# Optimization experiments

Measured on AMD Instinct MI355X. Metric: run time of the kernel, lower is better.

The kernel has to match this reference:

```python
import jax, jax.numpy as jnp
import numpy as np


def setup_inputs() -> dict:
    key = jax.random.key(0)
    ks = jax.random.split(key, 4)
    B, T, D, H = 64, 512, 512, 1024
    return {
        "x": jax.random.normal(ks[0], (B, T, D), dtype=jnp.float32),
        "kz": jax.random.normal(ks[1], (D, H), dtype=jnp.float32) * (1.0 / np.sqrt(D)),
        "kr": jax.random.normal(ks[2], (D, H), dtype=jnp.float32) * (1.0 / np.sqrt(D)),
        "kh": jax.random.normal(ks[3], (D, H), dtype=jnp.float32) * (1.0 / np.sqrt(D)),
        "mz": jnp.ones((H,), dtype=jnp.float32),
        "mr": jnp.ones((H,), dtype=jnp.float32),
        "br": jnp.zeros((H,), dtype=jnp.float32),
        "bz": jnp.zeros((H,), dtype=jnp.float32),
    }


def reference(x, kz, kr, kh, mz, mr, br, bz):
    B, T, D = x.shape
    H = kz.shape[1]
    # Precompute input projections for all timesteps (batched GEMMs),
    # identical math to per-step matmuls in the original cell.
    xz = jnp.einsum("btd,dh->bth", x, kz)  # [B,T,H]
    xr = jnp.einsum("btd,dh->bth", x, kr)
    xh = jnp.einsum("btd,dh->bth", x, kh)

    def step(h, inp):
        xz_t, xr_t, xh_t = inp  # each [B,H]
        r = jnp.tanh(xr_t + h * mr + br) + 1.0
        z = jax.nn.sigmoid(xz_t + h * mz + bz)
        h_new = z * h + (1.0 - z) * jnp.tanh(xh_t + r * h)
        return h_new, h_new

    h0 = jnp.zeros((B, H), dtype=x.dtype)
    # scan over time axis: move T to leading dim
    xs = (jnp.swapaxes(xz, 0, 1), jnp.swapaxes(xr, 0, 1), jnp.swapaxes(xh, 0, 1))
    _, ys = jax.lax.scan(step, h0, xs)  # ys: [T,B,H]
    return jnp.swapaxes(ys, 0, 1)  # [B,T,H]
```

## Files before the change

### kernel.cpp

```cpp
#include <hip/hip_runtime.h>
#include <hip/hip_bf16.h>
#include <math.h>


#define M_DIM 32768
#define K_DIM 512
#define H_DIM 1024
#define N3    3072

typedef _Float16 half8v __attribute__((ext_vector_type(8)));
typedef _Float16 half4v __attribute__((ext_vector_type(4)));
typedef float f32x4 __attribute__((ext_vector_type(4)));

__device__ __forceinline__ f32x4 mfma16(half8v a, half8v b, f32x4 c) {
    return __builtin_amdgcn_mfma_f32_16x16x32_f16(a, b, c, 0, 0, 0);
}

__device__ __forceinline__ void load_lds16(const void* g, void* l) {
    __builtin_amdgcn_global_load_lds(
        (const __attribute__((address_space(1))) void*)g,
        (__attribute__((address_space(3))) void*)l, 16, 0, 0);
}

__global__ __launch_bounds__(256) void convert_x(
    const float4* __restrict__ x4, half4v* __restrict__ hi4,
    half4v* __restrict__ lo4, int n4)
{
    int i = blockIdx.x * 256 + threadIdx.x;
    if (i >= n4) return;
    float4 v = x4[i];
    half4v h, lo;
    h.x = (_Float16)v.x; lo.x = (_Float16)(v.x - (float)h.x);
    h.y = (_Float16)v.y; lo.y = (_Float16)(v.y - (float)h.y);
    h.z = (_Float16)v.z; lo.z = (_Float16)(v.z - (float)h.z);
    h.w = (_Float16)v.w; lo.w = (_Float16)(v.w - (float)h.w);
    hi4[i] = h; lo4[i] = lo;
}

__global__ __launch_bounds__(256) void convert_wt(
    const float* __restrict__ kz, const float* __restrict__ kr,
    const float* __restrict__ kh, _Float16* __restrict__ wth,
    _Float16* __restrict__ wtl)
{
    int gid = blockIdx.x * 256 + threadIdx.x;
    int k = gid & (K_DIM - 1);
    int n = (gid >> 9) & (H_DIM - 1);
    int wsel = gid >> 19;
    const float* s = (wsel == 0) ? kz : ((wsel == 1) ? kr : kh);
    float v = s[(size_t)k * H_DIM + n];
    _Float16 h = (_Float16)v;
    wth[gid] = h;
    wtl[gid] = (_Float16)(v - (float)h);
}

__global__ __launch_bounds__(256) void gemm_mfma_split(
    const _Float16* __restrict__ Ahi, const _Float16* __restrict__ Alo,
    const _Float16* __restrict__ Bthi, const _Float16* __restrict__ Btlo,
    float* __restrict__ XZ, float* __restrict__ XR, float* __restrict__ OUT)
{
    __shared__ _Float16 Ah[128 * 32];
    __shared__ _Float16 Al[128 * 32];
    __shared__ _Float16 Bh[128 * 32];
    __shared__ _Float16 Bl[128 * 32];

    const int tid = threadIdx.x;
    const int w = tid >> 6, l = tid & 63;
    const int l15 = l & 15, quad = l >> 4;
    const int bx = blockIdx.x, by = blockIdx.y;
    const long m0 = (long)by * 128;
    const long n0 = (long)bx * 128;

    f32x4 acc[4][4] = {};

    const int s1 = tid, s2 = tid + 256;
    const long aoff1 = (m0 + (s1 >> 2)) * K_DIM + (s1 & 3) * 8;
    const long aoff2 = (m0 + (s2 >> 2)) * K_DIM + (s2 & 3) * 8;
    const long boff1 = (n0 + (s1 >> 2)) * K_DIM + (s1 & 3) * 8;
    const long boff2 = (n0 + (s2 >> 2)) * K_DIM + (s2 & 3) * 8;

    const _Float16* a1 = Ahi + aoff1;  const _Float16* a2 = Ahi + aoff2;
    const _Float16* q1 = Alo + aoff1;  const _Float16* q2 = Alo + aoff2;
    const _Float16* b1 = Bthi + boff1; const _Float16* b2 = Bthi + boff2;
    const _Float16* c1 = Btlo + boff1; const _Float16* c2 = Btlo + boff2;

    _Float16* ldsA1 = &Ah[w * 512]; _Float16* ldsA2 = &Ah[2048 + w * 512];
    _Float16* ldsQ1 = &Al[w * 512]; _Float16* ldsQ2 = &Al[2048 + w * 512];
    _Float16* ldsB1 = &Bh[w * 512]; _Float16* ldsB2 = &Bh[2048 + w * 512];
    _Float16* ldsC1 = &Bl[w * 512]; _Float16* ldsC2 = &Bl[2048 + w * 512];

    const int wm = (w >> 1) * 64, wn = (w & 1) * 64;

    for (int kk = 0; kk < K_DIM / 32; ++kk) {
        load_lds16(a1, ldsA1); load_lds16(a2, ldsA2);
        load_lds16(q1, ldsQ1); load_lds16(q2, ldsQ2);
        load_lds16(b1, ldsB1); load_lds16(b2, ldsB2);
        load_lds16(c1, ldsC1); load_lds16(c2, ldsC2);
        a1 += 32; a2 += 32; q1 += 32; q2 += 32;
        b1 += 32; b2 += 32; c1 += 32; c2 += 32;
        __syncthreads();

        half8v afh[4], afl[4], bfh[4], bfl[4];
#pragma unroll
        for (int mi = 0; mi < 4; ++mi) {
            int row = (wm + mi * 16 + l15) * 32 + quad * 8;
            afh[mi] = *(const half8v*)&Ah[row];
            afl[mi] = *(const half8v*)&Al[row];
        }
#pragma unroll
        for (int ni = 0; ni < 4; ++ni) {
            int row = (wn + ni * 16 + l15) * 32 + quad * 8;
            bfh[ni] = *(const half8v*)&Bh[row];
            bfl[ni] = *(const half8v*)&Bl[row];
        }
#pragma unroll
        for (int mi = 0; mi < 4; ++mi)
#pragma unroll
            for (int ni = 0; ni < 4; ++ni) {
                acc[mi][ni] = mfma16(afh[mi], bfh[ni], acc[mi][ni]);
                acc[mi][ni] = mfma16(afh[mi], bfl[ni], acc[mi][ni]);
                acc[mi][ni] = mfma16(afl[mi], bfh[ni], acc[mi][ni]);
            }
        __syncthreads();
    }

    float* dst = (bx < 8) ? XZ : ((bx < 16) ? XR : OUT);
    const long nl = (long)(bx & 7) * 128 + wn + l15;
#pragma unroll
    for (int mi = 0; mi < 4; ++mi) {
        const long m = m0 + wm + mi * 16 + quad * 4;
#pragma unroll
        for (int ni = 0; ni < 4; ++ni) {
            float* p = dst + m * H_DIM + nl + ni * 16;
#pragma unroll
            for (int i = 0; i < 4; ++i)
                p[(long)i * H_DIM] = acc[mi][ni][i];
        }
    }
}

#define BM 128
#define BN 128
#define BK 8
__global__ __launch_bounds__(256) void gemm_f32(
    const float* __restrict__ A, const float* __restrict__ B,
    float* __restrict__ C, int M, int N, int K)
{
    __shared__ float As[BK][BM];
    __shared__ float Bs[BK][BN];
    const int tid = threadIdx.x;
    const int bm = blockIdx.y * BM, bn = blockIdx.x * BN;
    const int tx = tid & 15, ty = tid >> 4;
    float acc[8][8];
#pragma unroll
    for (int i = 0; i < 8; i++)
#pragma unroll
        for (int j = 0; j < 8; j++) acc[i][j] = 0.f;
    const int a_row = tid >> 1, a_k = (tid & 1) * 4;
    const int b_row = tid >> 5, b_col = (tid & 31) * 4;
    const float* Aptr = A + (size_t)(bm + a_row) * K + a_k;
    const float* Bptr = B + (size_t)b_row * N + bn + b_col;
    for (int k0 = 0; k0 < K; k0 += BK) {
        float4 av = *(const float4*)(Aptr + k0);
        float4 bv = *(const float4*)(Bptr + (size_t)k0 * N);
        As[a_k + 0][a_row] = av.x; As[a_k + 1][a_row] = av.y;
        As[a_k + 2][a_row] = av.z; As[a_k + 3][a_row] = av.w;
        *(float4*)&Bs[b_row][b_col] = bv;
        __syncthreads();
#pragma unroll
        for (int kk = 0; kk < BK; kk++) {
            float4 a0 = *(const float4*)&As[kk][ty * 8];
            float4 a1 = *(const float4*)&As[kk][ty * 8 + 4];
            float4 b0 = *(const float4*)&Bs[kk][tx * 8];
            float4 b1 = *(const float4*)&Bs[kk][tx * 8 + 4];
            float a[8] = {a0.x, a0.y, a0.z, a0.w, a1.x, a1.y, a1.z, a1.w};
            float b[8] = {b0.x, b0.y, b0.z, b0.w, b1.x, b1.y, b1.z, b1.w};
#pragma unroll
            for (int i = 0; i < 8; i++)
#pragma unroll
                for (int j = 0; j < 8; j++)
                    acc[i][j] = fmaf(a[i], b[j], acc[i][j]);
        }
        __syncthreads();
    }
    float* Cptr = C + (size_t)(bm + ty * 8) * N + bn + tx * 8;
#pragma unroll
    for (int i = 0; i < 8; i++) {
        float4 c0 = {acc[i][0], acc[i][1], acc[i][2], acc[i][3]};
        float4 c1 = {acc[i][4], acc[i][5], acc[i][6], acc[i][7]};
        *(float4*)(Cptr + (size_t)i * N)     = c0;
        *(float4*)(Cptr + (size_t)i * N + 4) = c1;
    }
}

__device__ __forceinline__ float fast_tanh(float x) {
    return 1.0f - 2.0f / (__expf(2.0f * x) + 1.0f);
}
__device__ __forceinline__ float fast_sigmoid(float x) {
    return 1.0f / (1.0f + __expf(-x));
}

__global__ __launch_bounds__(256) void scan_kernel(
    const float* __restrict__ XZ, const float* __restrict__ XR,
    float* __restrict__ OUT,
    const float* __restrict__ mz, const float* __restrict__ mr,
    const float* __restrict__ br, const float* __restrict__ bz)
{
    const int gid = blockIdx.x * blockDim.x + threadIdx.x;
    const int b = gid >> 10;
    const int h = gid & (H_DIM - 1);

    const float mzv = mz[h], mrv = mr[h], brv = br[h], bzv = bz[h];
    float hs = 0.f;
    size_t idx = (size_t)b * 512 * H_DIM + h;

    float cz[8], cr[8], ch[8];
#pragma unroll
    for (int j = 0; j < 8; ++j) {
        cz[j] = XZ[idx + (size_t)j * H_DIM];
        cr[j] = XR[idx + (size_t)j * H_DIM];
        ch[j] = OUT[idx + (size_t)j * H_DIM];
    }
    for (int t0 = 0; t0 < 512; t0 += 8) {
        float nz[8], nr[8], nh[8];
        const bool more = (t0 + 8) < 512;
        const size_t nidx = idx + 8ul * H_DIM;
        if (more) {
#pragma unroll
            for (int j = 0; j < 8; ++j) {
                nz[j] = XZ[nidx + (size_t)j * H_DIM];
                nr[j] = XR[nidx + (size_t)j * H_DIM];
                nh[j] = OUT[nidx + (size_t)j * H_DIM];
            }
        }
#pragma unroll
        for (int j = 0; j < 8; ++j) {
            const float r = fast_tanh(fmaf(hs, mrv, cr[j]) + brv) + 1.0f;
            const float z = fast_sigmoid(fmaf(hs, mzv, cz[j]) + bzv);
            const float hn = fmaf(z, hs, (1.0f - z) * fast_tanh(fmaf(r, hs, ch[j])));
            OUT[idx + (size_t)j * H_DIM] = hn;
            hs = hn;
        }
        idx = nidx;
        if (more) {
#pragma unroll
            for (int j = 0; j < 8; ++j) { cz[j] = nz[j]; cr[j] = nr[j]; ch[j] = nh[j]; }
        }
    }
}

extern "C" void kernel_launch(void* const* d_in, const int* in_sizes, int n_in,
                              void* d_out, int out_size, void* d_ws, size_t ws_size,
                              hipStream_t stream) {
    const float* x  = (const float*)d_in[0];
    const float* kz = (const float*)d_in[1];
    const float* kr = (const float*)d_in[2];
    const float* kh = (const float*)d_in[3];
    const float* mz = (const float*)d_in[4];
    const float* mr = (const float*)d_in[5];
    const float* br = (const float*)d_in[6];
    const float* bz = (const float*)d_in[7];
    float* out = (float*)d_out;

    char* ws = (char*)d_ws;
    float* XZ = (float*)ws;
    float* XR = (float*)(ws + 134217728ul);
    _Float16* XHI = (_Float16*)(ws + 268435456ul);
    _Float16* XLO = (_Float16*)(ws + 301989888ul);
    _Float16* WTH = (_Float16*)(ws + 335544320ul);
    _Float16* WTL = (_Float16*)(ws + 338690048ul);
    const size_t need = 341835776ul;

    if (ws_size >= need) {
        int n4 = M_DIM * K_DIM / 4;
        convert_x<<<n4 / 256, 256, 0, stream>>>(
            (const float4*)x, (half4v*)XHI, (half4v*)XLO, n4);
        convert_wt<<<(3 * H_DIM * K_DIM) / 256, 256, 0, stream>>>(
            kz, kr, kh, WTH, WTL);
        dim3 grid(N3 / 128, M_DIM / 128);
        gemm_mfma_split<<<grid, 256, 0, stream>>>(
            XHI, XLO, WTH, WTL, XZ, XR, out);
    } else {
        dim3 grid(H_DIM / BN, M_DIM / BM);
        gemm_f32<<<grid, 256, 0, stream>>>(x, kz, XZ,  M_DIM, H_DIM, K_DIM);
        gemm_f32<<<grid, 256, 0, stream>>>(x, kr, XR,  M_DIM, H_DIM, K_DIM);
        gemm_f32<<<grid, 256, 0, stream>>>(x, kh, out, M_DIM, H_DIM, K_DIM);
    }

    scan_kernel<<<(64 * H_DIM) / 256, 256, 0, stream>>>(
        XZ, XR, out, mz, mr, br, bz);
}
```

Measured before the change: 613.4 us.

## Swizzle GEMM LDS layout, remap blocks for XCD locality, deepen scan prefetch

The split-fp16 GEMM now packs the hi and lo halves into combined 64-wide LDS rows with an XOR swizzle, to cut bank conflicts on fragment reads. It also launches a 1D grid and remaps block ids so that consecutive blocks on each of 8 groups cover nearby tiles, aiming for better L2 reuse across XCDs. Separately, the scan kernel's register prefetch depth is raised from 8 to 16 timesteps to hide more memory latency, at the cost of more registers and possibly lower occupancy.

```diff
diff --git a/kernel.cpp b/kernel.cpp
--- a/kernel.cpp
+++ b/kernel.cpp
@@ -58,59 +58,64 @@
     const _Float16* __restrict__ Bthi, const _Float16* __restrict__ Btlo,
     float* __restrict__ XZ, float* __restrict__ XR, float* __restrict__ OUT)
 {
-    __shared__ _Float16 Ah[128 * 32];
-    __shared__ _Float16 Al[128 * 32];
-    __shared__ _Float16 Bh[128 * 32];
-    __shared__ _Float16 Bl[128 * 32];
+    __shared__ _Float16 AT[128 * 64];
+    __shared__ _Float16 BT[128 * 64];
 
     const int tid = threadIdx.x;
     const int w = tid >> 6, l = tid & 63;
     const int l15 = l & 15, quad = l >> 4;
-    const int bx = blockIdx.x, by = blockIdx.y;
+
+    const int nblk = blockIdx.x;
+    const int swz = (nblk & 7) * 768 + (nblk >> 3);
+    const int by = swz / 24;
+    const int bx = swz - by * 24;
     const long m0 = (long)by * 128;
     const long n0 = (long)bx * 128;
 
     f32x4 acc[4][4] = {};
 
-    const int s1 = tid, s2 = tid + 256;
-    const long aoff1 = (m0 + (s1 >> 2)) * K_DIM + (s1 & 3) * 8;
-    const long aoff2 = (m0 + (s2 >> 2)) * K_DIM + (s2 & 3) * 8;
-    const long boff1 = (n0 + (s1 >> 2)) * K_DIM + (s1 & 3) * 8;
-    const long boff2 = (n0 + (s2 >> 2)) * K_DIM + (s2 & 3) * 8;
-
-    const _Float16* a1 = Ahi + aoff1;  const _Float16* a2 = Ahi + aoff2;
-    const _Float16* q1 = Alo + aoff1;  const _Float16* q2 = Alo + aoff2;
-    const _Float16* b1 = Bthi + boff1; const _Float16* b2 = Bthi + boff2;
-    const _Float16* c1 = Btlo + boff1; const _Float16* c2 = Btlo + boff2;
-
-    _Float16* ldsA1 = &Ah[w * 512]; _Float16* ldsA2 = &Ah[2048 + w * 512];
-    _Float16* ldsQ1 = &Al[w * 512]; _Float16* ldsQ2 = &Al[2048 + w * 512];
-    _Float16* ldsB1 = &Bh[w * 512]; _Float16* ldsB2 = &Bh[2048 + w * 512];
-    _Float16* ldsC1 = &Bl[w * 512]; _Float16* ldsC2 = &Bl[2048 + w * 512];
+    const _Float16* gsrc[8];
+    _Float16* ldst[8];
+#pragma unroll
+    for (int i = 0; i < 8; ++i) {
+        const int sb = w * 64 + (i & 3) * 256;
+        const int s  = sb + l;
+        const int r  = s >> 3;
+        const int o2 = ((s & 7) ^ (r & 7)) << 4;
+        const int part  = o2 >> 6;
+        const int khalf = ((o2 >> 4) & 3) * 8;
+        const bool isB = (i >= 4);
+        const long grow = (isB ? n0 : m0) + r;
+        const _Float16* base =
+            isB ? (part ? Btlo : Bthi) : (part ? Alo : Ahi);
+        gsrc[i] = base + grow * K_DIM + khalf;
+        ldst[i] = (isB ? BT : AT) + sb * 8;
+    }
 
     const int wm = (w >> 1) * 64, wn = (w & 1) * 64;
 
     for (int kk = 0; kk < K_DIM / 32; ++kk) {
-        load_lds16(a1, ldsA1); load_lds16(a2, ldsA2);
-        load_lds16(q1, ldsQ1); load_lds16(q2, ldsQ2);
-        load_lds16(b1, ldsB1); load_lds16(b2, ldsB2);
-        load_lds16(c1, ldsC1); load_lds16(c2, ldsC2);
-        a1 += 32; a2 += 32; q1 += 32; q2 += 32;
-        b1 += 32; b2 += 32; c1 += 32; c2 += 32;
+#pragma unroll
+        for (int i = 0; i < 8; ++i) {
+            load_lds16(gsrc[i], ldst[i]);
+            gsrc[i] += 32;
+        }
         __syncthreads();
 
         half8v afh[4], afl[4], bfh[4], bfl[4];
 #pragma unroll
         for (int mi = 0; mi < 4; ++mi) {
-            int row = (wm + mi * 16 + l15) * 32 + quad * 8;
-            afh[mi] = *(const half8v*)&Ah[row];
-            afl[mi] = *(const half8v*)&Al[row];
+            const int r = wm + mi * 16 + l15;
+            const int off = (quad ^ (r & 7)) * 8;
+            afh[mi] = *(const half8v*)&AT[r * 64 + off];
+            afl[mi] = *(const half8v*)&AT[r * 64 + (off ^ 32)];
         }
 #pragma unroll
         for (int ni = 0; ni < 4; ++ni) {
-            int row = (wn + ni * 16 + l15) * 32 + quad * 8;
-            bfh[ni] = *(const half8v*)&Bh[row];
-            bfl[ni] = *(const half8v*)&Bl[row];
+            const int r = wn + ni * 16 + l15;
+            const int off = (quad ^ (r & 7)) * 8;
+            bfh[ni] = *(const half8v*)&BT[r * 64 + off];
+            bfl[ni] = *(const half8v*)&BT[r * 64 + (off ^ 32)];
         }
 #pragma unroll
         for (int mi = 0; mi < 4; ++mi)
@@ -213,27 +218,27 @@
     float hs = 0.f;
     size_t idx = (size_t)b * 512 * H_DIM + h;
 
-    float cz[8], cr[8], ch[8];
-#pragma unroll
-    for (int j = 0; j < 8; ++j) {
+    float cz[16], cr[16], ch[16];
+#pragma unroll
+    for (int j = 0; j < 16; ++j) {
         cz[j] = XZ[idx + (size_t)j * H_DIM];
         cr[j] = XR[idx + (size_t)j * H_DIM];
         ch[j] = OUT[idx + (size_t)j * H_DIM];
     }
-    for (int t0 = 0; t0 < 512; t0 += 8) {
-        float nz[8], nr[8], nh[8];
-        const bool more = (t0 + 8) < 512;
-        const size_t nidx = idx + 8ul * H_DIM;
+    for (int t0 = 0; t0 < 512; t0 += 16) {
+        float nz[16], nr[16], nh[16];
+        const bool more = (t0 + 16) < 512;
+        const size_t nidx = idx + 16ul * H_DIM;
         if (more) {
 #pragma unroll
-            for (int j = 0; j < 8; ++j) {
+            for (int j = 0; j < 16; ++j) {
                 nz[j] = XZ[nidx + (size_t)j * H_DIM];
                 nr[j] = XR[nidx + (size_t)j * H_DIM];
                 nh[j] = OUT[nidx + (size_t)j * H_DIM];
             }
         }
 #pragma unroll
-        for (int j = 0; j < 8; ++j) {
+        for (int j = 0; j < 16; ++j) {
             const float r = fast_tanh(fmaf(hs, mrv, cr[j]) + brv) + 1.0f;
             const float z = fast_sigmoid(fmaf(hs, mzv, cz[j]) + bzv);
             const float hn = fmaf(z, hs, (1.0f - z) * fast_tanh(fmaf(r, hs, ch[j])));
@@ -243,7 +248,7 @@
         idx = nidx;
         if (more) {
 #pragma unroll
-            for (int j = 0; j < 8; ++j) { cz[j] = nz[j]; cr[j] = nr[j]; ch[j] = nh[j]; }
+            for (int j = 0; j < 16; ++j) { cz[j] = nz[j]; cr[j] = nr[j]; ch[j] = nh[j]; }
         }
     }
 }
@@ -276,8 +281,7 @@
             (const float4*)x, (half4v*)XHI, (half4v*)XLO, n4);
         convert_wt<<<(3 * H_DIM * K_DIM) / 256, 256, 0, stream>>>(
             kz, kr, kh, WTH, WTL);
-        dim3 grid(N3 / 128, M_DIM / 128);
-        gemm_mfma_split<<<grid, 256, 0, stream>>>(
+        gemm_mfma_split<<<6144, 256, 0, stream>>>(
             XHI, XLO, WTH, WTL, XZ, XR, out);
     } else {
         dim3 grid(H_DIM / BN, M_DIM / BM);
```

New measurement: 612.2 us. Within noise of the previous version (-0.2%).

## Store GEMM projections time-contiguous per (b,h) and vectorize scan loads

Applied to the files above, without the earlier changes.

The GEMM epilogue now writes the projections in a [B,H,T] layout, so each scan thread reads its own time series with contiguous float4 loads instead of strided per-step loads. The scan kernel folds the bias and gate constants into the preloaded values, prefetches 32 steps at a time, and replaces the divisions with rcp plus one Newton step. The weight conversion now transposes through shared memory to get coalesced accesses. This path needs an extra 128MB workspace buffer, and the transposed epilogue writes 16-byte chunks that are strided by 2KB.

```diff
diff --git a/kernel.cpp b/kernel.cpp
--- a/kernel.cpp
+++ b/kernel.cpp
@@ -37,22 +37,47 @@
     hi4[i] = h; lo4[i] = lo;
 }
 
-__global__ __launch_bounds__(256) void convert_wt(
+__global__ __launch_bounds__(256) void convert_wt_t(
     const float* __restrict__ kz, const float* __restrict__ kr,
     const float* __restrict__ kh, _Float16* __restrict__ wth,
     _Float16* __restrict__ wtl)
 {
-    int gid = blockIdx.x * 256 + threadIdx.x;
-    int k = gid & (K_DIM - 1);
-    int n = (gid >> 9) & (H_DIM - 1);
-    int wsel = gid >> 19;
-    const float* s = (wsel == 0) ? kz : ((wsel == 1) ? kr : kh);
-    float v = s[(size_t)k * H_DIM + n];
-    _Float16 h = (_Float16)v;
-    wth[gid] = h;
-    wtl[gid] = (_Float16)(v - (float)h);
-}
-
+    __shared__ float lds[64][65];
+    const int bid = blockIdx.x;
+    const int w = bid >> 7;
+    const int rem = bid & 127;
+    const int k0 = (rem >> 4) * 64;
+    const int n0 = (rem & 15) * 64;
+    const int tid = threadIdx.x;
+    const float* s = (w == 0) ? kz : ((w == 1) ? kr : kh);
+
+#pragma unroll
+    for (int r = 0; r < 4; ++r) {
+        const int kk = (tid >> 4) + r * 16;
+        const int nn = (tid & 15) * 4;
+        float4 v = *(const float4*)&s[(size_t)(k0 + kk) * H_DIM + n0 + nn];
+        lds[kk][nn + 0] = v.x; lds[kk][nn + 1] = v.y;
+        lds[kk][nn + 2] = v.z; lds[kk][nn + 3] = v.w;
+    }
+    __syncthreads();
+#pragma unroll
+    for (int r = 0; r < 4; ++r) {
+        const int nr = (tid >> 4) + r * 16;
+        const int kb = (tid & 15) * 4;
+        half4v hi, lo;
+#pragma unroll
+        for (int i = 0; i < 4; ++i) {
+            float v = lds[kb + i][nr];
+            _Float16 h = (_Float16)v;
+            hi[i] = h; lo[i] = (_Float16)(v - (float)h);
+        }
+        const size_t o = ((size_t)(w * H_DIM + n0 + nr)) * K_DIM + k0 + kb;
+        *(half4v*)&wth[o] = hi;
+        *(half4v*)&wtl[o] = lo;
+    }
+}
+
+template<bool TR>
 __global__ __launch_bounds__(256) void gemm_mfma_split(
     const _Float16* __restrict__ Ahi, const _Float16* __restrict__ Alo,
     const _Float16* __restrict__ Bthi, const _Float16* __restrict__ Btlo,
@@ -123,17 +148,32 @@
         __syncthreads();
     }
 
-    float* dst = (bx < 8) ? XZ : ((bx < 16) ? XR : OUT);
-    const long nl = (long)(bx & 7) * 128 + wn + l15;
-#pragma unroll
-    for (int mi = 0; mi < 4; ++mi) {
-        const long m = m0 + wm + mi * 16 + quad * 4;
-#pragma unroll
-        for (int ni = 0; ni < 4; ++ni) {
-            float* p = dst + m * H_DIM + nl + ni * 16;
-#pragma unroll
-            for (int i = 0; i < 4; ++i)
-                p[(long)i * H_DIM] = acc[mi][ni][i];
+    if (!TR) {
+        float* dst = (bx < 8) ? XZ : ((bx < 16) ? XR : OUT);
+        const long nl = (long)(bx & 7) * 128 + wn + l15;
+#pragma unroll
+        for (int mi = 0; mi < 4; ++mi) {
+            const long m = m0 + wm + mi * 16 + quad * 4;
+#pragma unroll
+            for (int ni = 0; ni < 4; ++ni) {
+                float* p = dst + m * H_DIM + nl + ni * 16;
+#pragma unroll
+                for (int i = 0; i < 4; ++i)
+                    p[(long)i * H_DIM] = acc[mi][ni][i];
+            }
+        }
+    } else {
+        float* dst = (bx < 8) ? XZ : ((bx < 16) ? XR : OUT);
+#pragma unroll
+        for (int mi = 0; mi < 4; ++mi) {
+            const long m = m0 + wm + mi * 16 + quad * 4;
+            const long b = m >> 9;
+            const long t = m & 511;
+#pragma unroll
+            for (int ni = 0; ni < 4; ++ni) {
+                const long n = (long)(bx & 7) * 128 + wn + ni * 16 + l15;
+                *(f32x4*)&dst[((size_t)(b * H_DIM + n) << 9) + t] = acc[mi][ni];
+            }
         }
     }
 }
@@ -192,11 +232,86 @@
     }
 }
 
-__device__ __forceinline__ float fast_tanh(float x) {
-    return 1.0f - 2.0f / (__expf(2.0f * x) + 1.0f);
-}
-__device__ __forceinline__ float fast_sigmoid(float x) {
-    return 1.0f / (1.0f + __expf(-x));
+__device__ __forceinline__ float vrcp_nr(float d) {
+    float r = __builtin_amdgcn_rcpf(d);
+    return r * fmaf(-d, r, 2.0f);
+}
+
+__global__ __launch_bounds__(256) void scan_t(
+    const float* __restrict__ XZt, const float* __restrict__ XRt,
+    const float* __restrict__ XHt, float* __restrict__ out,
+    const float* __restrict__ mz, const float* __restrict__ mr,
+    const float* __restrict__ br, const float* __restrict__ bz)
+{
+    const int gid = blockIdx.x * blockDim.x + threadIdx.x;
+    const int b = gid >> 10;
+    const int h = gid & (H_DIM - 1);
+
+    const float mzK = -mz[h];
+    const float mrK = -2.0f * mr[h];
+    const float bzK = -bz[h];
+    const float brK = -2.0f * br[h];
+    float hs = 0.f;
+
+    const size_t sbase = ((size_t)(b * H_DIM + h)) << 9;
+    const float4* pz = (const float4*)(XZt + sbase);
+    const float4* pr = (const float4*)(XRt + sbase);
+    const float4* ph = (const float4*)(XHt + sbase);
+    float* const po = out + ((size_t)b << 19) + h;
+
+    float cz[32], cr[32], ch[32];
+#pragma unroll
+    for (int q = 0; q < 8; ++q) {
+        float4 vz = pz[q], vr = pr[q], vh = ph[q];
+        cz[q*4+0] = bzK - vz.x; cz[q*4+1] = bzK - vz.y;
+        cz[q*4+2] = bzK - vz.z; cz[q*4+3] = bzK - vz.w;
+        cr[q*4+0] = fmaf(-2.0f, vr.x, brK); cr[q*4+1] = fmaf(-2.0f, vr.y, brK);
+        cr[q*4+2] = fmaf(-2.0f, vr.z, brK); cr[q*4+3] = fmaf(-2.0f, vr.w, brK);
+        ch[q*4+0] = -2.0f * vh.x; ch[q*4+1] = -2.0f * vh.y;
+        ch[q*4+2] = -2.0f * vh.z; ch[q*4+3] = -2.0f * vh.w;
+    }
+    for (int t0 = 0; t0 < 512; t0 += 32) {
+        float4 nz4[8], nr4[8], nh4[8];
+        const bool more = (t0 + 32) < 512;
+        if (more) {
+            const int b4 = (t0 + 32) >> 2;
+#pragma unroll
+            for (int q = 0; q < 8; ++q) {
+                nz4[q] = pz[b4 + q]; nr4[q] = pr[b4 + q]; nh4[q] = ph[b4 + q];
+            }
+        }
+        float* pout = po + ((size_t)t0 << 10);
+#pragma unroll
+        for (int j = 0; j < 32; ++j) {
+            const float u1   = fmaf(hs, mrK, cr[j]);
+            const float uz   = fmaf(hs, mzK, cz[j]);
+            const float hsK2 = -4.0f * hs;
+            const float e1 = __expf(u1);
+            const float s1 = vrcp_nr(e1 + 1.0f);
+            const float ez = __expf(uz);
+            const float sz = vrcp_nr(ez + 1.0f);
+            const float u2 = fmaf(s1, hsK2, ch[j]);
+            const float e2 = __expf(u2);
+            const float s2 = vrcp_nr(e2 + 1.0f);
+            const float th = fmaf(2.0f, s2, -1.0f);
+            const float hn = fmaf(sz, hs - th, th);
+            *pout = hn; pout += H_DIM;
+            hs = hn;
+        }
+        if (more) {
+#pragma unroll
+            for (int q = 0; q < 8; ++q) {
+                cz[q*4+0] = bzK - nz4[q].x; cz[q*4+1] = bzK - nz4[q].y;
+                cz[q*4+2] = bzK - nz4[q].z; cz[q*4+3] = bzK - nz4[q].w;
+                cr[q*4+0] = fmaf(-2.0f, nr4[q].x, brK);
+                cr[q*4+1] = fmaf(-2.0f, nr4[q].y, brK);
+                cr[q*4+2] = fmaf(-2.0f, nr4[q].z, brK);
+                cr[q*4+3] = fmaf(-2.0f, nr4[q].w, brK);
+                ch[q*4+0] = -2.0f * nh4[q].x; ch[q*4+1] = -2.0f * nh4[q].y;
+                ch[q*4+2] = -2.0f * nh4[q].z; ch[q*4+3] = -2.0f * nh4[q].w;
+            }
+        }
+    }
 }
 
 __global__ __launch_bounds__(256) void scan_kernel(
@@ -209,41 +324,57 @@
     const int b = gid >> 10;
     const int h = gid & (H_DIM - 1);
 
-    const float mzv = mz[h], mrv = mr[h], brv = br[h], bzv = bz[h];
+    const float mzK = -mz[h];
+    const float mrK = -2.0f * mr[h];
+    const float bzK = -bz[h];
+    const float brK = -2.0f * br[h];
     float hs = 0.f;
     size_t idx = (size_t)b * 512 * H_DIM + h;
 
-    float cz[8], cr[8], ch[8];
-#pragma unroll
-    for (int j = 0; j < 8; ++j) {
-        cz[j] = XZ[idx + (size_t)j * H_DIM];
-        cr[j] = XR[idx + (size_t)j * H_DIM];
-        ch[j] = OUT[idx + (size_t)j * H_DIM];
-    }
-    for (int t0 = 0; t0 < 512; t0 += 8) {
-        float nz[8], nr[8], nh[8];
-        const bool more = (t0 + 8) < 512;
-        const size_t nidx = idx + 8ul * H_DIM;
+    float cz[16], cr[16], ch[16];
+#pragma unroll
+    for (int j = 0; j < 16; ++j) {
+        cz[j] = bzK - XZ[idx + (size_t)j * H_DIM];
+        cr[j] = fmaf(-2.0f, XR[idx + (size_t)j * H_DIM], brK);
+        ch[j] = -2.0f * OUT[idx + (size_t)j * H_DIM];
+    }
+    for (int t0 = 0; t0 < 512; t0 += 16) {
+        float nz[16], nr[16], nh[16];
+        const bool more = (t0 + 16) < 512;
+        const size_t nidx = idx + 16ul * H_DIM;
         if (more) {
 #pragma unroll
-            for (int j = 0; j < 8; ++j) {
+            for (int j = 0; j < 16; ++j) {
                 nz[j] = XZ[nidx + (size_t)j * H_DIM];
                 nr[j] = XR[nidx + (size_t)j * H_DIM];
                 nh[j] = OUT[nidx + (size_t)j * H_DIM];
             }
         }
 #pragma unroll
-        for (int j = 0; j < 8; ++j) {
-            const float r = fast_tanh(fmaf(hs, mrv, cr[j]) + brv) + 1.0f;
-            const float z = fast_sigmoid(fmaf(hs, mzv, cz[j]) + bzv);
-            const float hn = fmaf(z, hs, (1.0f - z) * fast_tanh(fmaf(r, hs, ch[j])));
+        for (int j = 0; j < 16; ++j) {
+            const float u1   = fmaf(hs, mrK, cr[j]);
+            const float uz   = fmaf(hs, mzK, cz[j]);
+            const float hsK2 = -4.0f * hs;
+            const float e1 = __expf(u1);
+            const float s1 = vrcp_nr(e1 + 1.0f);
+            const float ez = __expf(uz);
+            const float sz = vrcp_nr(ez + 1.0f);
+            const float u2 = fmaf(s1, hsK2, ch[j]);
+            const float e2 = __expf(u2);
+            const float s2 = vrcp_nr(e2 + 1.0f);
+            const float th = fmaf(2.0f, s2, -1.0f);
+            const float hn = fmaf(sz, hs - th, th);
             OUT[idx + (size_t)j * H_DIM] = hn;
             hs = hn;
         }
         idx = nidx;
         if (more) {
 #pragma unroll
-            for (int j = 0; j < 8; ++j) { cz[j] = nz[j]; cr[j] = nr[j]; ch[j] = nh[j]; }
+            for (int j = 0; j < 16; ++j) {
+                cz[j] = bzK - nz[j];
+                cr[j] = fmaf(-2.0f, nr[j], brK);
+                ch[j] = -2.0f * nh[j];
+            }
         }
     }
 }
@@ -262,30 +393,52 @@
     float* out = (float*)d_out;
 
     char* ws = (char*)d_ws;
-    float* XZ = (float*)ws;
-    float* XR = (float*)(ws + 134217728ul);
-    _Float16* XHI = (_Float16*)(ws + 268435456ul);
-    _Float16* XLO = (_Float16*)(ws + 301989888ul);
-    _Float16* WTH = (_Float16*)(ws + 335544320ul);
-    _Float16* WTL = (_Float16*)(ws + 338690048ul);
-    const size_t need = 341835776ul;
-
-    if (ws_size >= need) {
-        int n4 = M_DIM * K_DIM / 4;
+    const int n4 = M_DIM * K_DIM / 4;
+
+    const size_t need_t = 476053504ul;
+    const size_t need_o = 341835776ul;
+
+    if (ws_size >= need_t) {
+        float* XZt = (float*)ws;
+        float* XRt = (float*)(ws + 134217728ul);
+        float* XHt = (float*)(ws + 268435456ul);
+        _Float16* XHI = (_Float16*)(ws + 402653184ul);
+        _Float16* XLO = (_Float16*)(ws + 436207616ul);
+        _Float16* WTH = (_Float16*)(ws + 469762048ul);
+        _Float16* WTL = (_Float16*)(ws + 472907776ul);
+
         convert_x<<<n4 / 256, 256, 0, stream>>>(
             (const float4*)x, (half4v*)XHI, (half4v*)XLO, n4);
-        convert_wt<<<(3 * H_DIM * K_DIM) / 256, 256, 0, stream>>>(
-            kz, kr, kh, WTH, WTL);
+        convert_wt_t<<<384, 256, 0, stream>>>(kz, kr, kh, WTH, WTL);
         dim3 grid(N3 / 128, M_DIM / 128);
-        gemm_mfma_split<<<grid, 256, 0, stream>>>(
+        gemm_mfma_split<true><<<grid, 256, 0, stream>>>(
+            XHI, XLO, WTH, WTL, XZt, XRt, XHt);
+        scan_t<<<(64 * H_DIM) / 256, 256, 0, stream>>>(
+            XZt, XRt, XHt, out, mz, mr, br, bz);
+    } else if (ws_size >= need_o) {
+        float* XZ = (float*)ws;
+        float* XR = (float*)(ws + 134217728ul);
+        _Float16* XHI = (_Float16*)(ws + 268435456ul);
+        _Float16* XLO = (_Float16*)(ws + 301989888ul);
+        _Float16* WTH = (_Float16*)(ws + 335544320ul);
+        _Float16* WTL = (_Float16*)(ws + 338690048ul);
+
+        convert_x<<<n4 / 256, 256, 0, stream>>>(
+            (const float4*)x, (half4v*)XHI, (half4v*)XLO, n4);
+        convert_wt_t<<<384, 256, 0, stream>>>(kz, kr, kh, WTH, WTL);
+        dim3 grid(N3 / 128, M_DIM / 128);
+        gemm_mfma_split<false><<<grid, 256, 0, stream>>>(
             XHI, XLO, WTH, WTL, XZ, XR, out);
+        scan_kernel<<<(64 * H_DIM) / 256, 256, 0, stream>>>(
+            XZ, XR, out, mz, mr, br, bz);
     } else {
+        float* XZ = (float*)ws;
+        float* XR = (float*)(ws + 134217728ul);
         dim3 grid(H_DIM / BN, M_DIM / BM);
         gemm_f32<<<grid, 256, 0, stream>>>(x, kz, XZ,  M_DIM, H_DIM, K_DIM);
         gemm_f32<<<grid, 256, 0, stream>>>(x, kr, XR,  M_DIM, H_DIM, K_DIM);
         gemm_f32<<<grid, 256, 0, stream>>>(x, kh, out, M_DIM, H_DIM, K_DIM);
-    }
-
-    scan_kernel<<<(64 * H_DIM) / 256, 256, 0, stream>>>(
-        XZ, XR, out, mz, mr, br, bz);
-}
+        scan_kernel<<<(64 * H_DIM) / 256, 256, 0, stream>>>(
+            XZ, XR, out, mz, mr, br, bz);
+    }
+}
```

After: 601.6 us. No clear change (-1.9%).
